# Kernel tuning notes

Measured on AMD Instinct MI355X. Metric: run time of the kernel, lower is better.

## Reference

```python
import jax, jax.numpy as jnp
import numpy as np

BT = 64  # chunk size

def _l2norm(x, eps=1e-6):
    n = jnp.linalg.norm(x, axis=-1, keepdims=True)
    return x / jnp.maximum(n, eps)

def _kda_gate(g_raw, A_log, dt_bias):
    # g = -exp(A_log) * softplus(g_raw + dt_bias); broadcast A_log over K
    return -jnp.exp(A_log)[None, None, :, None] * jax.nn.softplus(g_raw.astype(jnp.float32) + dt_bias[None, None].astype(jnp.float32))

def _chunk_kda_fwd(q, k, v, g, beta):
    B, T, H, K = q.shape
    V = v.shape[-1]
    assert T % BT == 0
    NT = T // BT
    scale = K ** -0.5
    q = _l2norm(q.astype(jnp.float32)) * scale
    k = _l2norm(k.astype(jnp.float32))

    def to_chunks(x, d):
        # [B,T,H,d] -> [NT,B,H,BT,d]
        return x.astype(jnp.float32).transpose(0, 2, 1, 3).reshape(B, H, NT, BT, d).transpose(2, 0, 1, 3, 4)

    qc, kc, vc, gc = to_chunks(q, K), to_chunks(k, K), to_chunks(v, V), to_chunks(g, K)
    bc = beta.astype(jnp.float32).transpose(0, 2, 1).reshape(B, H, NT, BT).transpose(2, 0, 1, 3)  # [NT,B,H,BT]

    eye = jnp.eye(BT, dtype=jnp.float32)
    tril_strict = jnp.tril(jnp.ones((BT, BT), bool), -1)
    tril_incl = jnp.tril(jnp.ones((BT, BT), bool), 0)

    def body(S, xs):
        q_i, k_i, v_i, g_i, b_i = xs  # [B,H,BT,*]
        gcum = jnp.cumsum(g_i, axis=-2)                              # [B,H,BT,K]
        diff = gcum[:, :, :, None, :] - gcum[:, :, None, :, :]      # [B,H,BT,BT,K]
        decay = jnp.exp(jnp.minimum(diff, 0.0))
        # intra-chunk k-k matrix, beta row-scaled, strictly lower, negated
        Akk = jnp.einsum('bhik,bhjk,bhijk->bhij', k_i, k_i, decay)
        M = -jnp.where(tril_strict, Akk * b_i[..., :, None], 0.0)
        # UT transform: torch in-place loop solves Tm = (I - M)^{-1}
        Tm = jax.scipy.linalg.solve_triangular(eye - M, jnp.broadcast_to(eye, M.shape), lower=True)
        Afin = Tm * b_i[..., None, :]                                # column scale by beta
        k_eg = k_i * jnp.exp(gcum)
        w = Afin @ k_eg                                              # [B,H,BT,K]
        u = Afin @ v_i                                               # [B,H,BT,V]
        Aqk = jnp.einsum('bhik,bhjk,bhijk->bhij', q_i, k_i, decay)
        Aqk = jnp.where(tril_incl, Aqk, 0.0)
        v_new = u - w @ S
        o_i = (q_i * jnp.exp(gcum)) @ S + Aqk @ v_new
        g_last = gcum[:, :, -1, :]                                   # [B,H,K]
        k_dec = jnp.exp(g_last[:, :, None, :] - gcum) * k_i
        S_new = S * jnp.exp(g_last)[..., None] + jnp.einsum('bhck,bhcv->bhkv', k_dec, v_new)
        return S_new, o_i

    S0 = jnp.zeros((B, H, K, V), jnp.float32)
    _, o = jax.lax.scan(body, S0, (qc, kc, vc, gc, bc))              # o: [NT,B,H,BT,V]
    return o.transpose(1, 2, 0, 3, 4).reshape(B, H, T, V).transpose(0, 2, 1, 3)


def setup_inputs() -> dict:
    key = jax.random.key(0)
    ks = jax.random.split(key, 7)
    B, T, H, K, V = 2, 8192, 16, 32, 64
    return {
        'q': jax.random.normal(ks[0], (B, T, H, K), jnp.float32),
        'k': jax.random.normal(ks[1], (B, T, H, K), jnp.float32),
        'v': jax.random.normal(ks[2], (B, T, H, V), jnp.float32),
        'g_raw': jax.random.normal(ks[3], (B, T, H, K), jnp.float32),
        'beta': jax.random.uniform(ks[4], (B, T, H), jnp.float32),
        'A_log': jax.random.normal(ks[5], (H,), jnp.float32) - 3.0,  # moderate decay rate
        'dt_bias': jax.random.normal(ks[6], (H, K), jnp.float32) * 0.1,
    }


def reference(q, k, v, g_raw, beta, A_log, dt_bias):
    g = _kda_gate(g_raw, A_log, dt_bias)
    return _chunk_kda_fwd(q, k, v, g, beta)
```

## Files before the change

kernel.cpp:

```cpp
#include <hip/hip_runtime.h>
#include <math.h>

#define Tt 8192
#define Hh 16
#define NCH 4096

#define OFF_U   ((size_t)NCH*2048)
#define OFF_M   ((size_t)NCH*6144)
#define OFF_C   ((size_t)NCH*7168)
#define OFF_MS  ((size_t)NCH*9216)
#define OFF_CS  (OFF_MS + (size_t)256*1024)
#define OFF_SS  (OFF_CS + (size_t)256*2048)

__device__ __forceinline__ float softplusf(float x) {
  return fmaxf(x, 0.f) + log1pf(__expf(-fabsf(x)));
}


__global__ __launch_bounds__(256) void kda_phase1(
    const float* __restrict__ kin, const float* __restrict__ vin,
    const float* __restrict__ graw, const float* __restrict__ beta,
    const float* __restrict__ A_log, const float* __restrict__ dt_bias,
    float* __restrict__ ws)
{
  __shared__ float sG[64*33];
  __shared__ float sK[64*33];
  __shared__ float sU[2720];
  __shared__ float sW[3104];

  const int tid = threadIdx.x;
  const int ch = blockIdx.x;
  const int c = ch >> 5, bh = ch & 31;
  const int b = bh >> 4, h = bh & 15;
  const int t0 = c*64;
  const int iq = tid >> 2, kq = (tid & 3)*8;

  float* wsW = ws;
  float* wsU = ws + OFF_U;
  float* wsM = ws + OFF_M;
  float* wsCc= ws + OFF_C;

  const float negA = -__expf(A_log[h]);

  {
    const float* gr = graw + (((size_t)b*Tt + t0 + iq)*Hh + h)*32 + kq;
    const float* db = dt_bias + h*32 + kq;
    #pragma unroll
    for (int r = 0; r < 8; ++r)
      sG[iq*33 + kq + r] = negA * softplusf(gr[r] + db[r]);
  }
  __syncthreads();
  if (tid < 32) {
    float c0 = 0.f;
    for (int blk = 0; blk < 4; ++blk) {
      float v[16];
      #pragma unroll
      for (int i = 0; i < 16; ++i) v[i] = sG[(blk*16+i)*33 + tid];
      #pragma unroll
      for (int i = 0; i < 16; ++i) { c0 += v[i]; sG[(blk*16+i)*33 + tid] = c0; }
    }
  }
  {
    const float* kp = kin + (((size_t)b*Tt + t0 + iq)*Hh + h)*32 + kq;
    float kr[8]; float ss = 0.f;
    #pragma unroll
    for (int r = 0; r < 8; ++r) { kr[r] = kp[r]; ss += kr[r]*kr[r]; }
    ss += __shfl_xor(ss, 1); ss += __shfl_xor(ss, 2);
    const float sc = 1.f / fmaxf(sqrtf(ss), 1e-6f);
    #pragma unroll
    for (int r = 0; r < 8; ++r) sK[iq*33 + kq + r] = kr[r]*sc;
  }
  __syncthreads();

  const float b_cm = beta[((size_t)b*Tt + t0 + (tid & 63))*Hh + h];
  float* P  = sU;
  float* Qb = sU + 2304;
  const int i64 = tid & 63, jj2 = (tid >> 6)*2;
  const int pL = i64 >> 4, pLb = pL*(pL+1)/2, iL = i64 & 15;
  for (int jt = 0; jt < 8; ++jt) {
    const int j0 = jt*8;
    {
      float pv[8];
      #pragma unroll
      for (int r = 0; r < 8; ++r) {
        const int idx = iq*33 + kq + r;
        pv[r] = sK[idx] * __expf(fminf(sG[idx] - sG[j0*33 + kq + r], 0.f));
      }
      *(float4*)(P + iq*36 + kq)     = make_float4(pv[0],pv[1],pv[2],pv[3]);
      *(float4*)(P + iq*36 + kq + 4) = make_float4(pv[4],pv[5],pv[6],pv[7]);
    }
    {
      const int jj = tid >> 5, kk = tid & 31;
      Qb[jj*32 + kk] = sK[(j0+jj)*33 + kk] * __expf(sG[j0*33 + kk] - sG[(j0+jj)*33 + kk]);
    }
    __syncthreads();
    float a0 = 0.f, a1 = 0.f;
    #pragma unroll
    for (int hf = 0; hf < 2; ++hf) {
      const int k0 = hf*16;
      #pragma unroll
      for (int t4 = 0; t4 < 4; ++t4) {
        const float4 pa = *(const float4*)(P  + i64*36 + k0 + t4*4);
        const float4 xa = *(const float4*)(Qb + (jj2  )*32 + k0 + t4*4);
        const float4 xb = *(const float4*)(Qb + (jj2+1)*32 + k0 + t4*4);
        a0 += pa.x*xa.x + pa.y*xa.y + pa.z*xa.z + pa.w*xa.w;
        a1 += pa.x*xb.x + pa.y*xb.y + pa.z*xb.z + pa.w*xb.w;
      }
    }
    const int j_0 = j0 + jj2;
    const int qB = j_0 >> 4;
    if (pL >= qB) {
      float* Lb = sW + (pLb + qB)*256 + iL;
      Lb[((j_0  ) & 15)*16] = (i64 > j_0  ) ? a0*b_cm : 0.f;
      Lb[((j_0+1) & 15)*16] = (i64 > j_0+1) ? a1*b_cm : 0.f;
    }
    __syncthreads();
  }

  if (tid < 64) {
    const int p = tid >> 4, col = tid & 15;
    const int bD = p*(p+1)/2 + p;
    float* Td = sU + bD*272;
    const float* Ld = sW + bD*256;
    Td[col] = (col == 0) ? 1.f : 0.f;
    for (int i = 1; i < 16; ++i) {
      float acc = 0.f;
      for (int j = 0; j < i; ++j)
        acc -= Ld[j*16 + i] * Td[j*17 + col];
      Td[i*17 + col] = acc + ((i == col) ? 1.f : 0.f);
    }
  }
  __syncthreads();
  {
    const int wid = tid >> 6;
    const int lane = tid & 63;
    const int ri = lane & 15, c4 = (lane >> 4)*4;
    float* Ct = sW + 2560 + wid*272;
    auto offblk = [&](int p, int q) {
      const int pb = p*(p+1)/2;
      float a0=0.f, a1=0.f, a2=0.f, a3=0.f;
      for (int m = q; m < p; ++m) {
        const float* Lb = sW + (pb + m)*256;
        const float* Tb = sU + (m*(m+1)/2 + q)*272;
        #pragma unroll
        for (int j = 0; j < 16; ++j) {
          const float lv = Lb[j*16 + ri];
          const float* tp = Tb + j*17 + c4;
          a0 += lv*tp[0]; a1 += lv*tp[1]; a2 += lv*tp[2]; a3 += lv*tp[3];
        }
      }
      float* cp = Ct + ri*17 + c4;
      cp[0]=a0; cp[1]=a1; cp[2]=a2; cp[3]=a3;
      const float* Tpp = sU + (pb + p)*272 + ri*17;
      float b0=0.f, b1=0.f, b2=0.f, b3=0.f;
      #pragma unroll
      for (int j = 0; j < 16; ++j) {
        const float tv = Tpp[j];
        const float* cj = Ct + j*17 + c4;
        b0 += tv*cj[0]; b1 += tv*cj[1]; b2 += tv*cj[2]; b3 += tv*cj[3];
      }
      float* op = sU + (pb + q)*272 + ri*17 + c4;
      op[0]=-b0; op[1]=-b1; op[2]=-b2; op[3]=-b3;
    };
    if (wid == 0) offblk(1,0); else if (wid == 1) offblk(2,1);
    __syncthreads();
    if (wid == 0) offblk(2,0); else if (wid == 1) offblk(3,1);
    __syncthreads();
    if (wid == 0) offblk(3,0); else if (wid == 1) offblk(3,2);
  }
  __syncthreads();

  {
    const float b_row = beta[((size_t)b*Tt + t0 + iq)*Hh + h];
    #pragma unroll
    for (int r = 0; r < 8; ++r) {
      const int idx = iq*33 + kq + r;
      const float g = sG[idx], kn = sK[idx];
      sW[iq*32 + kq + r] = b_row * kn * __expf(g);
      sK[idx] = kn * __expf(sG[63*33 + kq + r] - g);
    }
    if (tid < 32) sW[3072 + tid] = __expf(sG[63*33 + tid]);
  }
  __syncthreads();

  const int pT = iq >> 4, pTb = pT*(pT+1)/2;
  const int r17 = (iq & 15)*17, iqm = iq & 15;

  {
    float acc[8] = {0,0,0,0,0,0,0,0};
    for (int m = 0; m <= pT; ++m) {
      const float* Tb = sU + (pTb + m)*272 + r17;
      const int jmax = (m == pT) ? iqm : 15;
      const float* eb = sW + m*16*32 + kq;
      for (int jj = 0; jj <= jmax; ++jj) {
        const float t = Tb[jj];
        const float4 e0 = *(const float4*)(eb + jj*32);
        const float4 e1 = *(const float4*)(eb + jj*32 + 4);
        acc[0]+=t*e0.x; acc[1]+=t*e0.y; acc[2]+=t*e0.z; acc[3]+=t*e0.w;
        acc[4]+=t*e1.x; acc[5]+=t*e1.y; acc[6]+=t*e1.z; acc[7]+=t*e1.w;
      }
    }
    #pragma unroll
    for (int r = 0; r < 8; ++r) {
      wsW[(size_t)ch*2048 + tid*8 + r] = acc[r];
      sG[iq*32 + kq + r] = acc[r];
    }
  }
  __syncthreads();

  const int vs8 = (tid & 3)*8;
  for (int vh = 0; vh < 2; ++vh) {
    {
      #pragma unroll
      for (int r = 0; r < 2; ++r) {
        const int f = tid + 256*r;
        const int j = f >> 3, cc = (f & 7)*4;
        const float bj = beta[((size_t)b*Tt + t0 + j)*Hh + h];
        float4 v4 = *(const float4*)(vin + (((size_t)b*Tt + t0 + j)*Hh + h)*64 + vh*32 + cc);
        v4.x *= bj; v4.y *= bj; v4.z *= bj; v4.w *= bj;
        *(float4*)(sW + j*32 + cc) = v4;
      }
    }
    __syncthreads();
    float ua[8];
    {
      #pragma unroll
      for (int r = 0; r < 8; ++r) ua[r] = 0.f;
      for (int m = 0; m <= pT; ++m) {
        const float* Tb = sU + (pTb + m)*272 + r17;
        const int jmax = (m == pT) ? iqm : 15;
        const float* eb = sW + m*16*32 + vs8;
        for (int jj = 0; jj <= jmax; ++jj) {
          const float t = Tb[jj];
          const float4 e0 = *(const float4*)(eb + jj*32);
          const float4 e1 = *(const float4*)(eb + jj*32 + 4);
          ua[0]+=t*e0.x; ua[1]+=t*e0.y; ua[2]+=t*e0.z; ua[3]+=t*e0.w;
          ua[4]+=t*e1.x; ua[5]+=t*e1.y; ua[6]+=t*e1.z; ua[7]+=t*e1.w;
        }
      }
      *(float4*)(wsU + (size_t)ch*4096 + iq*64 + vh*32 + vs8)     = make_float4(ua[0],ua[1],ua[2],ua[3]);
      *(float4*)(wsU + (size_t)ch*4096 + iq*64 + vh*32 + vs8 + 4) = make_float4(ua[4],ua[5],ua[6],ua[7]);
    }
    __syncthreads();
    *(float4*)(sW + iq*32 + vs8)     = make_float4(ua[0],ua[1],ua[2],ua[3]);
    *(float4*)(sW + iq*32 + vs8 + 4) = make_float4(ua[4],ua[5],ua[6],ua[7]);
    __syncthreads();
    if (vh == 0) {
      const int a = tid >> 3, b4 = (tid & 7)*4;
      float mA[4] = {0.f,0.f,0.f,0.f};
      for (int t = 0; t < 64; ++t) {
        const float kd = sK[t*33 + a];
        const float4 wv = *(const float4*)(sG + t*32 + b4);
        mA[0]+=kd*wv.x; mA[1]+=kd*wv.y; mA[2]+=kd*wv.z; mA[3]+=kd*wv.w;
      }
      const float eg = sW[3072 + a];
      float4 m4;
      m4.x = ((a == b4+0) ? eg : 0.f) - mA[0];
      m4.y = ((a == b4+1) ? eg : 0.f) - mA[1];
      m4.z = ((a == b4+2) ? eg : 0.f) - mA[2];
      m4.w = ((a == b4+3) ? eg : 0.f) - mA[3];
      *(float4*)(wsM + (size_t)ch*1024 + tid*4) = m4;
    }
    {
      const int a = tid >> 3, c4c = (tid & 7)*4;
      float cA[4] = {0.f,0.f,0.f,0.f};
      for (int t = 0; t < 64; ++t) {
        const float kd = sK[t*33 + a];
        const float4 u4 = *(const float4*)(sW + t*32 + c4c);
        cA[0]+=kd*u4.x; cA[1]+=kd*u4.y; cA[2]+=kd*u4.z; cA[3]+=kd*u4.w;
      }
      *(float4*)(wsCc + (size_t)ch*2048 + a*64 + vh*32 + c4c) = make_float4(cA[0],cA[1],cA[2],cA[3]);
    }
    __syncthreads();
  }
}

__global__ __launch_bounds__(256) void kda_scanA(float* __restrict__ ws)
{
  __shared__ float sMa[32*33];
  __shared__ float sMc[32*33];
  __shared__ float sCa[32*18];
  const int tid = threadIdx.x;
  const int vt = blockIdx.x & 3, seg = (blockIdx.x >> 2) & 7, bh = blockIdx.x >> 5;
  const int v0 = vt*16;
  const int a = tid >> 3, b4 = (tid & 7)*4, c2 = (tid & 7)*2;
  const float* wsM = ws + OFF_M;
  const float* wsC = ws + OFF_C;

  #pragma unroll
  for (int r = 0; r < 4; ++r) sMa[a*33 + b4 + r] = (a == b4 + r) ? 1.f : 0.f;
  sCa[a*18 + c2] = 0.f; sCa[a*18 + c2 + 1] = 0.f;

  int ch = (seg*16)*32 + bh;
  float4 m4 = *(const float4*)(wsM + (size_t)ch*1024 + tid*4);
  float2 cc = *(const float2*)(wsC + (size_t)ch*2048 + a*64 + v0 + c2);

  for (int i = 0; i < 16; ++i) {
    sMc[a*33+b4+0]=m4.x; sMc[a*33+b4+1]=m4.y; sMc[a*33+b4+2]=m4.z; sMc[a*33+b4+3]=m4.w;
    __syncthreads();
    float4 m4n = m4; float2 ccn = cc;
    if (i < 15) {
      const int chn = (seg*16 + i + 1)*32 + bh;
      m4n = *(const float4*)(wsM + (size_t)chn*1024 + tid*4);
      ccn = *(const float2*)(wsC + (size_t)chn*2048 + a*64 + v0 + c2);
    }
    float cn0 = cc.x, cn1 = cc.y;
    float mn0=0.f, mn1=0.f, mn2=0.f, mn3=0.f;
    for (int bb = 0; bb < 32; ++bb) {
      const float m = sMc[a*33 + bb];
      const float2 s2 = *(const float2*)(sCa + bb*18 + c2);
      cn0 += m*s2.x; cn1 += m*s2.y;
      mn0 += m*sMa[bb*33+b4+0]; mn1 += m*sMa[bb*33+b4+1];
      mn2 += m*sMa[bb*33+b4+2]; mn3 += m*sMa[bb*33+b4+3];
    }
    __syncthreads();
    sCa[a*18+c2] = cn0; sCa[a*18+c2+1] = cn1;
    sMa[a*33+b4+0]=mn0; sMa[a*33+b4+1]=mn1; sMa[a*33+b4+2]=mn2; sMa[a*33+b4+3]=mn3;
    m4 = m4n; cc = ccn;
  }
  const size_t sid = (size_t)(bh*8 + seg);
  float* wsMs = ws + OFF_MS;
  float* wsCs = ws + OFF_CS;
  if (vt == 0) {
    #pragma unroll
    for (int r = 0; r < 4; ++r) wsMs[sid*1024 + tid*4 + r] = sMa[a*33+b4+r];
  }
  float2 co; co.x = sCa[a*18+c2]; co.y = sCa[a*18+c2+1];
  *(float2*)(wsCs + sid*2048 + a*64 + v0 + c2) = co;
}

__global__ __launch_bounds__(256) void kda_scanB(float* __restrict__ ws)
{
  __shared__ float sS[32*18];
  __shared__ float sM[32*33];
  const int tid = threadIdx.x;
  const int vt = blockIdx.x & 3, bh = blockIdx.x >> 2;
  const int v0 = vt*16;
  const int a = tid >> 3, b4 = (tid & 7)*4, c2 = (tid & 7)*2;
  const float* wsMs = ws + OFF_MS;
  const float* wsCs = ws + OFF_CS;
  float* wsSs = ws + OFF_SS;

  float s0 = 0.f, s1 = 0.f;
  sS[a*18 + c2] = 0.f; sS[a*18 + c2 + 1] = 0.f;
  const size_t sid0 = (size_t)(bh*8);
  float4 m4 = *(const float4*)(wsMs + sid0*1024 + tid*4);
  float2 cc = *(const float2*)(wsCs + sid0*2048 + a*64 + v0 + c2);

  for (int seg = 0; seg < 8; ++seg) {
    const size_t sid = (size_t)(bh*8 + seg);
    *(float2*)(wsSs + sid*2048 + a*64 + v0 + c2) = make_float2(s0, s1);
    sM[a*33+b4+0]=m4.x; sM[a*33+b4+1]=m4.y; sM[a*33+b4+2]=m4.z; sM[a*33+b4+3]=m4.w;
    __syncthreads();
    float4 m4n = m4; float2 ccn = cc;
    if (seg < 7) {
      m4n = *(const float4*)(wsMs + (sid+1)*1024 + tid*4);
      ccn = *(const float2*)(wsCs + (sid+1)*2048 + a*64 + v0 + c2);
    }
    float n0 = cc.x, n1 = cc.y;
    for (int bb = 0; bb < 32; ++bb) {
      const float m = sM[a*33 + bb];
      const float2 s2 = *(const float2*)(sS + bb*18 + c2);
      n0 += m*s2.x; n1 += m*s2.y;
    }
    __syncthreads();
    s0 = n0; s1 = n1;
    sS[a*18+c2] = s0; sS[a*18+c2+1] = s1;
    m4 = m4n; cc = ccn;
  }
}

__global__ __launch_bounds__(256) void kda_scanC(float* __restrict__ ws)
{
  __shared__ float sM[32*33];
  __shared__ float sS[32*18];
  const int tid = threadIdx.x;
  const int vt = blockIdx.x & 3, seg = (blockIdx.x >> 2) & 7, bh = blockIdx.x >> 5;
  const int v0 = vt*16;
  const int a = tid >> 3, b4 = (tid & 7)*4, c2 = (tid & 7)*2;
  const float* wsM = ws + OFF_M;
  float* wsC = ws + OFF_C;
  const float* wsSs = ws + OFF_SS;

  const size_t sid = (size_t)(bh*8 + seg);
  float s0, s1;
  {
    float2 sv = *(const float2*)(wsSs + sid*2048 + a*64 + v0 + c2);
    s0 = sv.x; s1 = sv.y;
    sS[a*18 + c2] = s0; sS[a*18 + c2 + 1] = s1;
  }
  int ch = (seg*16)*32 + bh;
  float4 m4 = *(const float4*)(wsM + (size_t)ch*1024 + tid*4);
  float2 cc = *(const float2*)(wsC + (size_t)ch*2048 + a*64 + v0 + c2);

  for (int i = 0; i < 16; ++i) {
    const int chc = (seg*16 + i)*32 + bh;
    sM[a*33+b4+0]=m4.x; sM[a*33+b4+1]=m4.y; sM[a*33+b4+2]=m4.z; sM[a*33+b4+3]=m4.w;
    *(float2*)(wsC + (size_t)chc*2048 + a*64 + v0 + c2) = make_float2(s0, s1);
    __syncthreads();
    float4 m4n = m4; float2 ccn = cc;
    if (i < 15) {
      const int chn = (seg*16 + i + 1)*32 + bh;
      m4n = *(const float4*)(wsM + (size_t)chn*1024 + tid*4);
      ccn = *(const float2*)(wsC + (size_t)chn*2048 + a*64 + v0 + c2);
    }
    float n0 = cc.x, n1 = cc.y;
    for (int bb = 0; bb < 32; ++bb) {
      const float m = sM[a*33 + bb];
      const float2 s2 = *(const float2*)(sS + bb*18 + c2);
      n0 += m*s2.x; n1 += m*s2.y;
    }
    __syncthreads();
    s0 = n0; s1 = n1;
    sS[a*18+c2] = s0; sS[a*18+c2+1] = s1;
    m4 = m4n; cc = ccn;
  }
}

__global__ __launch_bounds__(256) void kda_phase3(
    const float* __restrict__ qin, const float* __restrict__ kin,
    const float* __restrict__ graw,
    const float* __restrict__ A_log, const float* __restrict__ dt_bias,
    const float* __restrict__ ws, float* __restrict__ out)
{
  __shared__ float sG[64*33];
  __shared__ float sQ[64*33];
  __shared__ float sA[2720];
  __shared__ float sV[2560];

  const int tid = threadIdx.x;
  const int ch = blockIdx.x;
  const int c = ch >> 5, bh = ch & 31;
  const int b = bh >> 4, h = bh & 15;
  const int t0 = c*64;
  const int iq = tid >> 2, kq = (tid & 3)*8;

  const float* wsW = ws;
  const float* wsU = ws + OFF_U;
  const float* wsS = ws + OFF_C;

  const float negA = -__expf(A_log[h]);
  {
    const float* gr = graw + (((size_t)b*Tt + t0 + iq)*Hh + h)*32 + kq;
    const float* db = dt_bias + h*32 + kq;
    #pragma unroll
    for (int r = 0; r < 8; ++r)
      sG[iq*33 + kq + r] = negA * softplusf(gr[r] + db[r]);
  }
  __syncthreads();
  if (tid < 32) {
    float c0 = 0.f;
    for (int blk = 0; blk < 4; ++blk) {
      float v[16];
      #pragma unroll
      for (int i = 0; i < 16; ++i) v[i] = sG[(blk*16+i)*33 + tid];
      #pragma unroll
      for (int i = 0; i < 16; ++i) { c0 += v[i]; sG[(blk*16+i)*33 + tid] = c0; }
    }
  }
  float knr[8];
  {
    const float* qp = qin + (((size_t)b*Tt + t0 + iq)*Hh + h)*32 + kq;
    float qr[8]; float ssq = 0.f;
    #pragma unroll
    for (int r = 0; r < 8; ++r) { qr[r] = qp[r]; ssq += qr[r]*qr[r]; }
    ssq += __shfl_xor(ssq, 1); ssq += __shfl_xor(ssq, 2);
    const float scq = 0.17677669529663687f / fmaxf(sqrtf(ssq), 1e-6f);
    #pragma unroll
    for (int r = 0; r < 8; ++r) sQ[iq*33 + kq + r] = qr[r]*scq;

    const float* kp = kin + (((size_t)b*Tt + t0 + iq)*Hh + h)*32 + kq;
    float ssk = 0.f;
    #pragma unroll
    for (int r = 0; r < 8; ++r) { knr[r] = kp[r]; ssk += knr[r]*knr[r]; }
    ssk += __shfl_xor(ssk, 1); ssk += __shfl_xor(ssk, 2);
    const float sck = 1.f / fmaxf(sqrtf(ssk), 1e-6f);
    #pragma unroll
    for (int r = 0; r < 8; ++r) knr[r] *= sck;
  }
  __syncthreads();

  float* P  = sV;
  float* Qb = sV + 2304;
  const int i64 = tid & 63, jj2 = (tid >> 6)*2;
  const int pL = i64 >> 4, pLb = pL*(pL+1)/2, iL = i64 & 15;
  for (int jt = 0; jt < 8; ++jt) {
    const int j0 = jt*8;
    {
      float pv[8];
      #pragma unroll
      for (int r = 0; r < 8; ++r) {
        const int idx = iq*33 + kq + r;
        pv[r] = sQ[idx] * __expf(fminf(sG[idx] - sG[j0*33 + kq + r], 0.f));
      }
      *(float4*)(P + iq*36 + kq)     = make_float4(pv[0],pv[1],pv[2],pv[3]);
      *(float4*)(P + iq*36 + kq + 4) = make_float4(pv[4],pv[5],pv[6],pv[7]);
    }
    if (iq >= j0 && iq < j0 + 8) {
      const int jj = iq - j0;
      #pragma unroll
      for (int r = 0; r < 8; ++r)
        Qb[jj*32 + kq + r] = knr[r] * __expf(sG[j0*33 + kq + r] - sG[iq*33 + kq + r]);
    }
    __syncthreads();
    float a0 = 0.f, a1 = 0.f;
    #pragma unroll
    for (int hf = 0; hf < 2; ++hf) {
      const int k0 = hf*16;
      #pragma unroll
      for (int t4 = 0; t4 < 4; ++t4) {
        const float4 pa = *(const float4*)(P  + i64*36 + k0 + t4*4);
        const float4 xa = *(const float4*)(Qb + (jj2  )*32 + k0 + t4*4);
        const float4 xb = *(const float4*)(Qb + (jj2+1)*32 + k0 + t4*4);
        a0 += pa.x*xa.x + pa.y*xa.y + pa.z*xa.z + pa.w*xa.w;
        a1 += pa.x*xb.x + pa.y*xb.y + pa.z*xb.z + pa.w*xb.w;
      }
    }
    const int j_0 = j0 + jj2;
    const int qB = j_0 >> 4;
    if (pL >= qB) {
      float* Ab = sA + (pLb + qB)*272 + iL*17;
      Ab[(j_0  ) & 15] = (i64 >= j_0  ) ? a0 : 0.f;
      Ab[(j_0+1) & 15] = (i64 >= j_0+1) ? a1 : 0.f;
    }
    __syncthreads();
  }

  float qgr[8];
  {
    #pragma unroll
    for (int r = 0; r < 8; ++r) {
      const int idx = iq*33 + kq + r;
      qgr[r] = sQ[idx] * __expf(sG[idx]);
    }
  }
  __syncthreads();
  {
    #pragma unroll
    for (int rr = 0; rr < 2; ++rr) {
      const int f = tid + 256*rr;
      *(float4*)(sG + f*4) = *(const float4*)(wsS + (size_t)ch*2048 + f*4);
    }
    *(float4*)(sV + tid*8)     = *(const float4*)(wsW + (size_t)ch*2048 + tid*8);
    *(float4*)(sV + tid*8 + 4) = *(const float4*)(wsW + (size_t)ch*2048 + tid*8 + 4);
  }
  __syncthreads();
  const int pT = iq >> 4, pTb = pT*(pT+1)/2;
  const int r17 = (iq & 15)*17, iqm = iq & 15;
  {
    float qe[8];
    #pragma unroll
    for (int r = 0; r < 8; ++r) qe[r] = qgr[r];
    for (int m = 0; m <= pT; ++m) {
      const float* Ab = sA + (pTb + m)*272 + r17;
      const int jmax = (m == pT) ? iqm : 15;
      const float* wb = sV + m*16*32 + kq;
      for (int jj = 0; jj <= jmax; ++jj) {
        const float av = Ab[jj];
        const float4 w0 = *(const float4*)(wb + jj*32);
        const float4 w1 = *(const float4*)(wb + jj*32 + 4);
        qe[0]-=av*w0.x; qe[1]-=av*w0.y; qe[2]-=av*w0.z; qe[3]-=av*w0.w;
        qe[4]-=av*w1.x; qe[5]-=av*w1.y; qe[6]-=av*w1.z; qe[7]-=av*w1.w;
      }
    }
    #pragma unroll
    for (int r = 0; r < 8; ++r) sQ[iq*33 + kq + r] = qe[r];
  }
  __syncthreads();

  const int vs8 = (tid & 3)*8;
  for (int vh = 0; vh < 2; ++vh) {
    {
      #pragma unroll
      for (int r = 0; r < 2; ++r) {
        const int f = tid + 256*r;
        const int j = f >> 3, ccu = (f & 7)*4;
        *(float4*)(sV + j*32 + ccu) = *(const float4*)(wsU + (size_t)ch*4096 + j*64 + vh*32 + ccu);
      }
    }
    __syncthreads();
    float acc[8];
    #pragma unroll
    for (int r = 0; r < 8; ++r) acc[r] = 0.f;
    {
      for (int kk = 0; kk < 32; ++kk) {
        const float qv = sQ[iq*33 + kk];
        const float* sb = sG + kk*64 + vh*32 + vs8;
        const float4 s0 = *(const float4*)sb;
        const float4 s1 = *(const float4*)(sb + 4);
        acc[0]+=qv*s0.x; acc[1]+=qv*s0.y; acc[2]+=qv*s0.z; acc[3]+=qv*s0.w;
        acc[4]+=qv*s1.x; acc[5]+=qv*s1.y; acc[6]+=qv*s1.z; acc[7]+=qv*s1.w;
      }
    }
    {
      for (int m = 0; m <= pT; ++m) {
        const float* Ab = sA + (pTb + m)*272 + r17;
        const int jmax = (m == pT) ? iqm : 15;
        const float* ub = sV + m*16*32 + vs8;
        for (int jj = 0; jj <= jmax; ++jj) {
          const float av = Ab[jj];
          const float4 u0 = *(const float4*)(ub + jj*32);
          const float4 u1 = *(const float4*)(ub + jj*32 + 4);
          acc[0]+=av*u0.x; acc[1]+=av*u0.y; acc[2]+=av*u0.z; acc[3]+=av*u0.w;
          acc[4]+=av*u1.x; acc[5]+=av*u1.y; acc[6]+=av*u1.z; acc[7]+=av*u1.w;
        }
      }
    }
    float* op = out + (((size_t)b*Tt + t0 + iq)*Hh + h)*64 + vh*32 + vs8;
    *(float4*)(op)     = make_float4(acc[0],acc[1],acc[2],acc[3]);
    *(float4*)(op + 4) = make_float4(acc[4],acc[5],acc[6],acc[7]);
    __syncthreads();
  }
}

extern "C" void kernel_launch(void* const* d_in, const int* in_sizes, int n_in,
                              void* d_out, int out_size, void* d_ws, size_t ws_size,
                              hipStream_t stream) {
  const float* q    = (const float*)d_in[0];
  const float* k    = (const float*)d_in[1];
  const float* v    = (const float*)d_in[2];
  const float* graw = (const float*)d_in[3];
  const float* beta = (const float*)d_in[4];
  const float* A_log= (const float*)d_in[5];
  const float* dtb  = (const float*)d_in[6];
  float* out = (float*)d_out;
  float* ws  = (float*)d_ws;

  kda_phase1<<<NCH, 256, 0, stream>>>(k, v, graw, beta, A_log, dtb, ws);
  kda_scanA<<<1024, 256, 0, stream>>>(ws);
  kda_scanB<<<128, 256, 0, stream>>>(ws);
  kda_scanC<<<1024, 256, 0, stream>>>(ws);
  kda_phase3<<<NCH, 256, 0, stream>>>(q, k, graw, A_log, dtb, ws, out);
}
```

Measured before the change: 578.1 us.

## Split output phase by row halves of U instead of V-column halves

The final output stage used to loop over two V-column halves, reloading the intra-chunk A coefficients and the q·S product for each half. It now gives each thread 16 output columns, loads U in two 32-row halves covering the full 64 columns, and computes q·S only once. Each A coefficient is therefore read once per row, and one barrier is removed. The cost is more registers per thread (16 accumulators), plus possible imbalance because row-halves contribute unequally across the causal triangle.

```diff
diff --git a/kernel.cpp b/kernel.cpp
--- a/kernel.cpp
+++ b/kernel.cpp
@@ -568,48 +568,57 @@
   }
   __syncthreads();
 
-  const int vs8 = (tid & 3)*8;
-  for (int vh = 0; vh < 2; ++vh) {
-    {
-      #pragma unroll
-      for (int r = 0; r < 2; ++r) {
-        const int f = tid + 256*r;
-        const int j = f >> 3, ccu = (f & 7)*4;
-        *(float4*)(sV + j*32 + ccu) = *(const float4*)(wsU + (size_t)ch*4096 + j*64 + vh*32 + ccu);
-      }
-    }
-    __syncthreads();
-    float acc[8];
-    #pragma unroll
-    for (int r = 0; r < 8; ++r) acc[r] = 0.f;
-    {
-      for (int kk = 0; kk < 32; ++kk) {
-        const float qv = sQ[iq*33 + kk];
-        const float* sb = sG + kk*64 + vh*32 + vs8;
-        const float4 s0 = *(const float4*)sb;
-        const float4 s1 = *(const float4*)(sb + 4);
-        acc[0]+=qv*s0.x; acc[1]+=qv*s0.y; acc[2]+=qv*s0.z; acc[3]+=qv*s0.w;
-        acc[4]+=qv*s1.x; acc[5]+=qv*s1.y; acc[6]+=qv*s1.z; acc[7]+=qv*s1.w;
-      }
-    }
-    {
-      for (int m = 0; m <= pT; ++m) {
+  {
+    const int vs = (tid & 3)*16;
+    float acc[16];
+    #pragma unroll
+    for (int r = 0; r < 16; ++r) acc[r] = 0.f;
+    for (int vh = 0; vh < 2; ++vh) {
+      {
+        #pragma unroll
+        for (int rr = 0; rr < 2; ++rr) {
+          const int f = tid + 256*rr;
+          *(float4*)(sV + f*4) = *(const float4*)(wsU + (size_t)ch*4096 + vh*2048 + f*4);
+        }
+      }
+      __syncthreads();
+      if (vh == 0) {
+        for (int kk = 0; kk < 32; ++kk) {
+          const float qv = sQ[iq*33 + kk];
+          const float4 s0 = *(const float4*)(sG + kk*64 + vs);
+          const float4 s1 = *(const float4*)(sG + kk*64 + vs + 4);
+          const float4 s2 = *(const float4*)(sG + kk*64 + vs + 8);
+          const float4 s3 = *(const float4*)(sG + kk*64 + vs + 12);
+          acc[0]+=qv*s0.x;  acc[1]+=qv*s0.y;  acc[2]+=qv*s0.z;  acc[3]+=qv*s0.w;
+          acc[4]+=qv*s1.x;  acc[5]+=qv*s1.y;  acc[6]+=qv*s1.z;  acc[7]+=qv*s1.w;
+          acc[8]+=qv*s2.x;  acc[9]+=qv*s2.y;  acc[10]+=qv*s2.z; acc[11]+=qv*s2.w;
+          acc[12]+=qv*s3.x; acc[13]+=qv*s3.y; acc[14]+=qv*s3.z; acc[15]+=qv*s3.w;
+        }
+      }
+      for (int m = vh*2; m <= pT && m < vh*2 + 2; ++m) {
         const float* Ab = sA + (pTb + m)*272 + r17;
         const int jmax = (m == pT) ? iqm : 15;
-        const float* ub = sV + m*16*32 + vs8;
+        const float* ub = sV + (m - vh*2)*16*64 + vs;
         for (int jj = 0; jj <= jmax; ++jj) {
           const float av = Ab[jj];
-          const float4 u0 = *(const float4*)(ub + jj*32);
-          const float4 u1 = *(const float4*)(ub + jj*32 + 4);
-          acc[0]+=av*u0.x; acc[1]+=av*u0.y; acc[2]+=av*u0.z; acc[3]+=av*u0.w;
-          acc[4]+=av*u1.x; acc[5]+=av*u1.y; acc[6]+=av*u1.z; acc[7]+=av*u1.w;
+          const float4 u0 = *(const float4*)(ub + jj*64);
+          const float4 u1 = *(const float4*)(ub + jj*64 + 4);
+          const float4 u2 = *(const float4*)(ub + jj*64 + 8);
+          const float4 u3 = *(const float4*)(ub + jj*64 + 12);
+          acc[0]+=av*u0.x;  acc[1]+=av*u0.y;  acc[2]+=av*u0.z;  acc[3]+=av*u0.w;
+          acc[4]+=av*u1.x;  acc[5]+=av*u1.y;  acc[6]+=av*u1.z;  acc[7]+=av*u1.w;
+          acc[8]+=av*u2.x;  acc[9]+=av*u2.y;  acc[10]+=av*u2.z; acc[11]+=av*u2.w;
+          acc[12]+=av*u3.x; acc[13]+=av*u3.y; acc[14]+=av*u3.z; acc[15]+=av*u3.w;
         }
       }
-    }
-    float* op = out + (((size_t)b*Tt + t0 + iq)*Hh + h)*64 + vh*32 + vs8;
-    *(float4*)(op)     = make_float4(acc[0],acc[1],acc[2],acc[3]);
-    *(float4*)(op + 4) = make_float4(acc[4],acc[5],acc[6],acc[7]);
-    __syncthreads();
+      if (vh == 0) __syncthreads();
+    }
+    float* op = out + (((size_t)b*Tt + t0 + iq)*Hh + h)*64 + vs;
+    #pragma unroll
+    for (int rr = 0; rr < 4; ++rr) {
+      float4 o4; o4.x=acc[rr*4]; o4.y=acc[rr*4+1]; o4.z=acc[rr*4+2]; o4.w=acc[rr*4+3];
+      *(float4*)(op + rr*4) = o4;
+    }
   }
 }
 
```

After: 534.9 us. 1.08x faster.
